# Performance work log

Measured on AMD Instinct MI355X. Metric: run time of the kernel, lower is better.

## Reference

```python
import jax, jax.numpy as jnp
import numpy as np

B, L, P, D = 2, 2048, 512, 4096
H, KH = 32, 8
HD = D // H  # 128
S = P + L


def setup_inputs() -> dict:
    key = jax.random.key(0)
    ks = jax.random.split(key, 8)
    x = jax.random.normal(ks[0], (B, L, D), dtype=jnp.float32)
    # causal mask accounting for past_len P: query i may attend keys j <= P + i
    qi = jnp.arange(L)[:, None]
    kj = jnp.arange(S)[None, :]
    mask = jnp.where(kj <= P + qi, 0.0, -1e9).astype(jnp.float32)[None, None]  # [1,1,L,S]
    past_k = jax.random.normal(ks[1], (B, KH, P, HD), dtype=jnp.float32)
    past_v = jax.random.normal(ks[2], (B, KH, P, HD), dtype=jnp.float32)
    scale = 0.02
    Wq = jax.random.normal(ks[3], (D, H * HD), dtype=jnp.float32) * scale
    Wk = jax.random.normal(ks[4], (D, KH * HD), dtype=jnp.float32) * scale
    Wv = jax.random.normal(ks[5], (D, KH * HD), dtype=jnp.float32) * scale
    Wo = jax.random.normal(ks[6], (D, D), dtype=jnp.float32) * scale
    return {"x": x, "mask": mask, "past_k": past_k, "past_v": past_v,
            "Wq": Wq, "Wk": Wk, "Wv": Wv, "Wo": Wo}


def reference(x, mask, past_k, past_v, Wq, Wk, Wv, Wo):
    b, l, d = x.shape
    # projections (nn.Linear with no bias: x @ W^T, here W stored already transposed)
    q = (x @ Wq).reshape(b, l, H, HD).transpose(0, 2, 1, 3)   # [B,H,L,hd]
    k = (x @ Wk).reshape(b, l, KH, HD).transpose(0, 2, 1, 3)  # [B,KH,L,hd]
    v = (x @ Wv).reshape(b, l, KH, HD).transpose(0, 2, 1, 3)
    # KV-cache concat along sequence dim
    k = jnp.concatenate([past_k, k], axis=2)  # [B,KH,S,hd]
    v = jnp.concatenate([past_v, v], axis=2)
    # GQA: repeat_interleave kv heads to match query heads
    g = H // KH
    k_rep = jnp.repeat(k, g, axis=1)  # [B,H,S,hd]
    v_rep = jnp.repeat(v, g, axis=1)
    scores = jnp.einsum('bhqd,bhkd->bhqk', q, k_rep) / (HD ** 0.5) + mask
    attn = jax.nn.softmax(scores, axis=-1)
    out = jnp.einsum('bhqk,bhkd->bhqd', attn, v_rep)
    out = out.transpose(0, 2, 1, 3).reshape(b, l, d) @ Wo
    return out
```

## Files before the change

### kernel.cpp

```cpp
#include <hip/hip_runtime.h>

using u16 = unsigned short;
using u32 = unsigned int;
using bf16x8 = __attribute__((ext_vector_type(8))) __bf16;
using f32x4  = __attribute__((ext_vector_type(4))) float;
using f32x16 = __attribute__((ext_vector_type(16))) float;
using u16x8  = __attribute__((ext_vector_type(8))) u16;
using u32x2  = __attribute__((ext_vector_type(2))) u32;

#define DEV static __device__ __forceinline__

DEV float bf2f(u16 u) { union { u32 i; float f; } c; c.i = ((u32)u) << 16; return c.f; }
DEV u16 f2bf(float f) {
  union { float f; u32 i; } c; c.f = f;
  u32 r = c.i + 0x7FFFu + ((c.i >> 16) & 1u);
  return (u16)(r >> 16);
}

DEV void gload_lds16(const void* g, void* l) {
  __builtin_amdgcn_global_load_lds(
      (const __attribute__((address_space(1))) u32*)g,
      (__attribute__((address_space(3))) u32*)l, 16, 0, 0);
}

DEV u32 cvtpk(float lo, float hi) {
  u32 r;
  asm("v_cvt_pk_bf16_f32 %0, %1, %2" : "=v"(r) : "v"(lo), "v"(hi));
  return r;
}
DEV void plswap(u32& a, u32& b) {
  auto r = __builtin_amdgcn_permlane32_swap((int)a, (int)b, false, false);
  a = (u32)r[0]; b = (u32)r[1];
}
DEV float crossmax(float x) {
  union { float f; u32 i; } c; c.f = x;
  u32 a = c.i, b = c.i;
  plswap(a, b);
  union { u32 i; float f; } A, B; A.i = a; B.i = b;
  return fmaxf(A.f, B.f);
}
DEV float crosssum(float x) {
  union { float f; u32 i; } c; c.f = x;
  u32 a = c.i, b = c.i;
  plswap(a, b);
  union { u32 i; float f; } A, B; A.i = a; B.i = b;
  return A.f + B.f;
}

DEV void fence_barrier() {
  asm volatile("" ::: "memory");
  __builtin_amdgcn_s_barrier();
  asm volatile("" ::: "memory");
}

__global__ __launch_bounds__(256) void cast_x_kernel(const float* __restrict__ x,
                                                     u16* __restrict__ xb) {
  size_t i = (size_t)blockIdx.x * 256 + threadIdx.x;
  const float4* s4 = (const float4*)(x + i * 8);
  float4 a = s4[0], c = s4[1];
  u16x8 o;
  o[0] = f2bf(a.x); o[1] = f2bf(a.y); o[2] = f2bf(a.z); o[3] = f2bf(a.w);
  o[4] = f2bf(c.x); o[5] = f2bf(c.y); o[6] = f2bf(c.z); o[7] = f2bf(c.w);
  *(u16x8*)(xb + i * 8) = o;
}

__global__ __launch_bounds__(256) void transpose_cast(const float* __restrict__ W,
                                                      u16* __restrict__ Wt, int K, int N) {
  __shared__ float t[32][33];
  int tx = threadIdx.x & 31, ty = threadIdx.x >> 5;
  int n0 = blockIdx.x * 32, k0 = blockIdx.y * 32;
#pragma unroll
  for (int i = 0; i < 4; ++i)
    t[ty + i * 8][tx] = W[(size_t)(k0 + ty + i * 8) * N + n0 + tx];
  __syncthreads();
#pragma unroll
  for (int i = 0; i < 4; ++i)
    Wt[(size_t)(n0 + ty + i * 8) * K + k0 + tx] = f2bf(t[tx][ty + i * 8]);
}


DEV int swap67(int p) { return (p & 63) | ((p & 64) << 1) | ((p & 128) >> 1); }
DEV int colmap(int p) { return (p & 31) | ((p & 96) << 1) | ((p >> 2) & 32); }

template <int PAR, int MH, int NH, bool VM, typename F>
DEV void gphase(const u16* lds, int wrp, int wcp, int c16, int g, int s7,
                f32x4 (&acc)[8][4], F&& stage) {
  bf16x8 af[4][2];
  bf16x8 bv[2][2];
#pragma unroll
  for (int fi = 0; fi < 4; ++fi) {
    const u16* rp = lds + PAR * 32768 + (MH * 128 + wrp + fi * 16 + c16) * 64;
    af[fi][0] = *(const bf16x8*)(rp + ((0 + g) ^ s7) * 8);
    af[fi][1] = *(const bf16x8*)(rp + ((4 + g) ^ s7) * 8);
  }
#pragma unroll
  for (int fj = 0; fj < 2; ++fj) {
    const u16* rp = lds + PAR * 32768 + 16384 + (NH * 128 + wcp + fj * 16 + c16) * 64;
    bv[fj][0] = *(const bf16x8*)(rp + ((0 + g) ^ s7) * 8);
    bv[fj][1] = *(const bf16x8*)(rp + ((4 + g) ^ s7) * 8);
  }
  stage();
  if (VM) asm volatile("s_waitcnt vmcnt(4)" ::: "memory");
  fence_barrier();
  __builtin_amdgcn_s_setprio(1);
#pragma unroll
  for (int fi = 0; fi < 4; ++fi)
#pragma unroll
    for (int fj = 0; fj < 2; ++fj) {
      acc[MH * 4 + fi][NH * 2 + fj] = __builtin_amdgcn_mfma_f32_16x16x32_bf16(
          af[fi][0], bv[fj][0], acc[MH * 4 + fi][NH * 2 + fj], 0, 0, 0);
      acc[MH * 4 + fi][NH * 2 + fj] = __builtin_amdgcn_mfma_f32_16x16x32_bf16(
          af[fi][1], bv[fj][1], acc[MH * 4 + fi][NH * 2 + fj], 0, 0, 0);
    }
  __builtin_amdgcn_s_setprio(0);
  fence_barrier();
}

template <typename CT>
__global__ __launch_bounds__(512, 2) void gemm8(const u16* __restrict__ A,
                                                const u16* __restrict__ Bt,
                                                CT* __restrict__ C, int M, int N, int K) {
  __shared__ u16 lds[65536];
  const int tid = threadIdx.x;
  const int w = tid >> 6, lane = tid & 63;
  const int g = lane >> 4, c16 = lane & 15, s7 = c16 & 7;
  const int nwg = gridDim.x * gridDim.y;
  const int bid0 = blockIdx.y * gridDim.x + blockIdx.x;
  const int sb = (bid0 & 7) * (nwg >> 3) + (bid0 >> 3);
  const int bn = (sb % gridDim.x) * 256;
  const int bm = (sb / gridDim.x) * 256;
  const int wr = (w >> 2) * 128, wc = (w & 3) * 64;
  const int wrp = (w >> 2) * 64, wcp = (w & 3) * 32;

  const int lr = lane >> 3;
  const int swz = ((lane & 7) ^ lr) * 8;
  u32 aOff[2][2], bOff[2][2];
#pragma unroll
  for (int h = 0; h < 2; ++h)
#pragma unroll
    for (int j = 0; j < 2; ++j) {
      int pb = h * 128 + (w * 2 + j) * 8;
      aOff[h][j] = (u32)(bm + swap67(pb) + lr) * (u32)K + swz;
      bOff[h][j] = (u32)(bn + colmap(pb) + lr) * (u32)K + swz;
    }
  auto stA = [&](int par, int h, int j, int ko) {
    gload_lds16(A + aOff[h][j] + ko, (u16*)lds + par * 32768 + h * 8192 + (w * 2 + j) * 512);
  };
  auto stB = [&](int par, int h, int j, int ko) {
    gload_lds16(Bt + bOff[h][j] + ko,
                (u16*)lds + par * 32768 + 16384 + h * 8192 + (w * 2 + j) * 512);
  };

  f32x4 acc[8][4] = {};

  stA(0, 0, 0, 0); stA(0, 0, 1, 0); stB(0, 0, 0, 0); stB(0, 0, 1, 0);
  stA(0, 1, 0, 0); stA(0, 1, 1, 0); stB(0, 1, 0, 0); stB(0, 1, 1, 0);
  stA(1, 0, 0, 64); stA(1, 0, 1, 64); stB(1, 0, 0, 64); stB(1, 0, 1, 64);
  asm volatile("s_waitcnt vmcnt(4)" ::: "memory");
  fence_barrier();

  for (int kb = 64; kb < K; kb += 128) {
    const int kc = kb + 64, kd = kb + 128;
    const bool hc = kc < K, hd = kd < K;
    gphase<0, 0, 0, false>(lds, wrp, wcp, c16, g, s7, acc, [&] {
      stA(1, 1, 0, kb); stA(1, 1, 1, kb); stB(1, 1, 0, kb); stB(1, 1, 1, kb);
    });
    gphase<0, 0, 1, false>(lds, wrp, wcp, c16, g, s7, acc, [&] {});
    gphase<0, 1, 0, false>(lds, wrp, wcp, c16, g, s7, acc, [&] {
      if (hc) { stA(0, 0, 0, kc); stA(0, 0, 1, kc); }
    });
    gphase<0, 1, 1, true>(lds, wrp, wcp, c16, g, s7, acc, [&] {
      if (hc) { stB(0, 0, 0, kc); stB(0, 0, 1, kc); }
    });
    gphase<1, 0, 0, false>(lds, wrp, wcp, c16, g, s7, acc, [&] {
      if (hc) { stA(0, 1, 0, kc); stA(0, 1, 1, kc); stB(0, 1, 0, kc); stB(0, 1, 1, kc); }
    });
    gphase<1, 0, 1, false>(lds, wrp, wcp, c16, g, s7, acc, [&] {});
    gphase<1, 1, 0, false>(lds, wrp, wcp, c16, g, s7, acc, [&] {
      if (hd) { stA(1, 0, 0, kd); stA(1, 0, 1, kd); }
    });
    gphase<1, 1, 1, true>(lds, wrp, wcp, c16, g, s7, acc, [&] {
      if (hd) { stB(1, 0, 0, kd); stB(1, 0, 1, kd); }
    });
  }

#pragma unroll
  for (int mf = 0; mf < 8; ++mf)
#pragma unroll
    for (int nf = 0; nf < 4; ++nf)
#pragma unroll
      for (int r = 0; r < 4; ++r) {
        int row = bm + wr + (mf >> 2) * 64 + (mf & 3) * 16 + g * 4 + r;
        int col = bn + wc + (nf >> 1) * 32 + (nf & 1) * 16 + c16;
        float v = acc[mf][nf][r];
        if constexpr (sizeof(CT) == 2) C[(size_t)row * N + col] = f2bf(v);
        else                           C[(size_t)row * N + col] = v;
      }
}

__global__ __launch_bounds__(256) void kcat(const float* __restrict__ past,
                                            const u16* __restrict__ kvb,
                                            u16* __restrict__ out) {
  int idx = blockIdx.x * 256 + threadIdx.x;
  int bkh = idx / 40960;
  int rem = idx - bkh * 40960;
  int s = rem >> 4;
  int d0 = (rem & 15) * 8;
  u16x8 o;
  if (s < 512) {
    const float4* s4 = (const float4*)(past + ((size_t)bkh * 512 + s) * 128 + d0);
    float4 a = s4[0], c = s4[1];
    o[0] = f2bf(a.x); o[1] = f2bf(a.y); o[2] = f2bf(a.z); o[3] = f2bf(a.w);
    o[4] = f2bf(c.x); o[5] = f2bf(c.y); o[6] = f2bf(c.z); o[7] = f2bf(c.w);
  } else {
    int b = bkh >> 3, khh = bkh & 7;
    o = *(const u16x8*)(kvb + (size_t)(b * 2048 + s - 512) * 2048 + khh * 128 + d0);
  }
  *(u16x8*)(out + (size_t)idx * 8) = o;
}

__global__ __launch_bounds__(256) void vt_build(const float* __restrict__ past,
                                                const u16* __restrict__ kvb,
                                                u16* __restrict__ vt) {
  __shared__ float t[32][33];
  int tx = threadIdx.x & 31, ty = threadIdx.x >> 5;
  int s0 = blockIdx.x * 32, d0 = blockIdx.y * 32, bkh = blockIdx.z;
  int b = bkh >> 3, khh = bkh & 7;
#pragma unroll
  for (int i = 0; i < 4; ++i) {
    int s = s0 + ty + i * 8;
    float v;
    if (s < 512) v = past[((size_t)bkh * 512 + s) * 128 + d0 + tx];
    else         v = bf2f(kvb[(size_t)(b * 2048 + s - 512) * 2048 + 1024 + khh * 128 + d0 + tx]);
    t[ty + i * 8][tx] = v;
  }
  __syncthreads();
#pragma unroll
  for (int i = 0; i < 4; ++i)
    vt[((size_t)bkh * 128 + d0 + ty + i * 8) * 2560 + s0 + tx] = f2bf(t[tx][ty + i * 8]);
}

__global__ __launch_bounds__(512, 2) void attn_fwd(const u16* __restrict__ Q,
                                                   const u16* __restrict__ Kc,
                                                   const u16* __restrict__ Vt,
                                                   u16* __restrict__ Oa) {
  __shared__ u16 lds[2][16384];
  const int tid = threadIdx.x;
  const int w = tid >> 6, lane = tid & 63;
  const int c32 = lane & 31, hi = lane >> 5;
  const int bid = blockIdx.x;
  const int b = bid >> 8;
  const int q8 = (bid >> 5) & 7;
  const int qt = b ? 7 - q8 : q8;
  const int h = bid & 31;
  const int kh = h >> 2;
  const int q0 = qt * 256;
  const int qw = q0 + w * 32;
  const int qg = qw + c32;
  const float SCALE = 0.08838834764831845f;

  bf16x8 qf[8];
  const u16* qbase = Q + (size_t)(b * 2048 + qg) * 4096 + h * 128 + hi * 8;
#pragma unroll
  for (int kc = 0; kc < 8; ++kc) qf[kc] = *(const bf16x8*)(qbase + kc * 16);

  const int krow = w * 4 + (lane >> 4);
  const int koff = krow * 128 + (((lane & 15) ^ (krow & 7)) * 8);
  const int vrow = w * 8 + (lane >> 3);
  const int voff = vrow * 2560 + (((lane & 7) ^ (vrow & 7)) * 8);
  const u16* kp = Kc + (size_t)(b * 8 + kh) * 2560 * 128;
  const u16* vp = Vt + (size_t)(b * 8 + kh) * 128 * 2560;
  u16* ksd0 = &lds[0][w * 512]; u16* ksd1 = &lds[1][w * 512];
  u16* vsd0 = &lds[0][8192 + w * 512]; u16* vsd1 = &lds[1][8192 + w * 512];

  const int ntiles = 4 * qt + 12;

  gload_lds16(kp + koff, ksd0);
  gload_lds16(kp + koff + 4096, ksd0 + 4096);
  gload_lds16(vp + voff, vsd0);
  gload_lds16(vp + voff + 163840, vsd0 + 4096);

  float m_run = -1e30f, l_run = 0.f;
  f32x16 oacc[4] = {};
  const int s7 = c32 & 7;

  for (int t = 0; t < ntiles; ++t) {
    const int pb = t & 1;
    if (t + 1 < ntiles) {
      u16* kd = pb ? ksd0 : ksd1;
      u16* vd = pb ? vsd0 : vsd1;
      gload_lds16(kp + 8192 + koff, kd);
      gload_lds16(kp + 8192 + koff + 4096, kd + 4096);
      gload_lds16(vp + 64 + voff, vd);
      gload_lds16(vp + 64 + voff + 163840, vd + 4096);
      asm volatile("s_waitcnt vmcnt(4)" ::: "memory");
    } else {
      asm volatile("s_waitcnt vmcnt(0)" ::: "memory");
    }
    __builtin_amdgcn_s_barrier();

    const int dd = 512 + qw - t * 64;
    if (dd >= -31) {
      const u16* Ks = &lds[pb][0];
      const u16* Vs = &lds[pb][8192];

      f32x16 sc[2] = {};
#pragma unroll
      for (int kc = 0; kc < 8; ++kc) {
#pragma unroll
        for (int sb = 0; sb < 2; ++sb) {
          const int sr = sb * 32 + c32;
          bf16x8 kf = *(const bf16x8*)(Ks + sr * 128 + (((kc * 2 + hi) ^ s7) * 8));
          sc[sb] = __builtin_amdgcn_mfma_f32_32x32x16_bf16(kf, qf[kc], sc[sb], 0, 0, 0);
        }
      }

      if (dd < 63) {
        const int base = 4 * hi - c32;
#pragma unroll
        for (int sb = 0; sb < 2; ++sb)
#pragma unroll
          for (int r = 0; r < 16; ++r) {
            const int srow = sb * 32 + (r & 3) + 8 * (r >> 2);
            if (srow + base > dd) sc[sb][r] = -1e30f;
          }
      }

      float pmax = -1e30f;
#pragma unroll
      for (int sb = 0; sb < 2; ++sb)
#pragma unroll
        for (int r = 0; r < 16; ++r) pmax = fmaxf(pmax, sc[sb][r]);
      pmax = crossmax(pmax);

      if (__any(pmax > m_run + 64.f)) {
        const float mn = fmaxf(m_run, pmax);
        const float corr = __expf((m_run - mn) * SCALE);
#pragma unroll
        for (int db = 0; db < 4; ++db)
#pragma unroll
          for (int r = 0; r < 16; ++r) oacc[db][r] *= corr;
        l_run *= corr;
        m_run = mn;
      }

      const float nms = -m_run * SCALE;
      float ls = 0.f;
#pragma unroll
      for (int sb = 0; sb < 2; ++sb)
#pragma unroll
        for (int r = 0; r < 16; ++r) {
          float p = __expf(fmaf(sc[sb][r], SCALE, nms));
          sc[sb][r] = p;
          ls += p;
        }
      l_run += crosssum(ls);

      bf16x8 pa[4];
#pragma unroll
      for (int c = 0; c < 4; ++c) {
        const int sb = c >> 1, bb = (c & 1) * 8;
        u32 a  = cvtpk(sc[sb][bb + 0], sc[sb][bb + 1]);
        u32 b2 = cvtpk(sc[sb][bb + 2], sc[sb][bb + 3]);
        u32 c2 = cvtpk(sc[sb][bb + 4], sc[sb][bb + 5]);
        u32 d2 = cvtpk(sc[sb][bb + 6], sc[sb][bb + 7]);
        plswap(a, c2);
        plswap(b2, d2);
        union { u32 u[4]; bf16x8 v; } cv;
        cv.u[0] = a; cv.u[1] = b2; cv.u[2] = c2; cv.u[3] = d2;
        pa[c] = cv.v;
      }

#pragma unroll
      for (int c = 0; c < 4; ++c) {
#pragma unroll
        for (int db = 0; db < 4; ++db) {
          const int d = db * 32 + c32;
          bf16x8 vf = *(const bf16x8*)(Vs + d * 64 + (((c * 2 + hi) ^ s7) * 8));
          oacc[db] = __builtin_amdgcn_mfma_f32_32x32x16_bf16(vf, pa[c], oacc[db], 0, 0, 0);
        }
      }
    }
    __builtin_amdgcn_s_barrier();
    kp += 8192; vp += 64;
  }

  const float linv = 1.f / l_run;
  u16* ob = Oa + (size_t)(b * 2048 + qg) * 4096 + h * 128 + 4 * hi;
#pragma unroll
  for (int db = 0; db < 4; ++db)
#pragma unroll
    for (int rg = 0; rg < 4; ++rg) {
      u32x2 st;
      st[0] = cvtpk(oacc[db][rg * 4 + 0] * linv, oacc[db][rg * 4 + 1] * linv);
      st[1] = cvtpk(oacc[db][rg * 4 + 2] * linv, oacc[db][rg * 4 + 3] * linv);
      *(u32x2*)(ob + db * 32 + rg * 8) = st;
    }
}

extern "C" void kernel_launch(void* const* d_in, const int* in_sizes, int n_in,
                              void* d_out, int out_size, void* d_ws, size_t ws_size,
                              hipStream_t stream) {
  (void)in_sizes; (void)n_in; (void)out_size; (void)ws_size;
  const float* x  = (const float*)d_in[0];
  const float* pk = (const float*)d_in[2];
  const float* pv = (const float*)d_in[3];
  const float* Wq = (const float*)d_in[4];
  const float* Wk = (const float*)d_in[5];
  const float* Wv = (const float*)d_in[6];
  const float* Wo = (const float*)d_in[7];
  float* out = (float*)d_out;

  char* w = (char*)d_ws;
  u16* xb  = (u16*)(w);
  u16* wt  = (u16*)(w + 33554432);
  u16* qb  = (u16*)(w + 67108864);
  u16* kvb = (u16*)(w + 100663296);
  u16* kc  = (u16*)(w + 117440512);
  u16* vt  = (u16*)(w + 127926272);
  u16* ao  = xb;

  cast_x_kernel<<<8192, 256, 0, stream>>>(x, xb);
  transpose_cast<<<dim3(128, 128), 256, 0, stream>>>(Wq, wt, 4096, 4096);
  gemm8<u16><<<dim3(16, 16), 512, 0, stream>>>(xb, wt, qb, 4096, 4096, 4096);
  transpose_cast<<<dim3(32, 128), 256, 0, stream>>>(Wk, wt, 4096, 1024);
  transpose_cast<<<dim3(32, 128), 256, 0, stream>>>(Wv, wt + (size_t)1024 * 4096, 4096, 1024);
  gemm8<u16><<<dim3(8, 16), 512, 0, stream>>>(xb, wt, kvb, 4096, 2048, 4096);
  kcat<<<2560, 256, 0, stream>>>(pk, kvb, kc);
  vt_build<<<dim3(80, 4, 16), 256, 0, stream>>>(pv, kvb, vt);
  transpose_cast<<<dim3(128, 128), 256, 0, stream>>>(Wo, wt, 4096, 4096);
  attn_fwd<<<512, 512, 0, stream>>>(qb, kc, vt, ao);
  gemm8<float><<<dim3(16, 16), 512, 0, stream>>>(ao, wt, out, 4096, 4096, 4096);
}
```

Before: 758.6 us.

## Split-K the KV projection GEMM and reuse LDS fragments across GEMM phases

After: 687.6 us. 9.4% less time.

```diff
diff --git a/kernel.cpp b/kernel.cpp
--- a/kernel.cpp
+++ b/kernel.cpp
@@ -82,22 +82,26 @@
 DEV int swap67(int p) { return (p & 63) | ((p & 64) << 1) | ((p & 128) >> 1); }
 DEV int colmap(int p) { return (p & 31) | ((p & 96) << 1) | ((p >> 2) & 32); }
 
-template <int PAR, int MH, int NH, bool VM, typename F>
+template <int PAR, int MH, int NH, bool LA, bool LB, bool VM, typename F>
 DEV void gphase(const u16* lds, int wrp, int wcp, int c16, int g, int s7,
-                f32x4 (&acc)[8][4], F&& stage) {
-  bf16x8 af[4][2];
-  bf16x8 bv[2][2];
-#pragma unroll
-  for (int fi = 0; fi < 4; ++fi) {
-    const u16* rp = lds + PAR * 32768 + (MH * 128 + wrp + fi * 16 + c16) * 64;
-    af[fi][0] = *(const bf16x8*)(rp + ((0 + g) ^ s7) * 8);
-    af[fi][1] = *(const bf16x8*)(rp + ((4 + g) ^ s7) * 8);
-  }
-#pragma unroll
-  for (int fj = 0; fj < 2; ++fj) {
-    const u16* rp = lds + PAR * 32768 + 16384 + (NH * 128 + wcp + fj * 16 + c16) * 64;
-    bv[fj][0] = *(const bf16x8*)(rp + ((0 + g) ^ s7) * 8);
-    bv[fj][1] = *(const bf16x8*)(rp + ((4 + g) ^ s7) * 8);
+                bf16x8 (&af)[4][2], bf16x8 (&bv)[2][2][2],
+                f32x4 (&acc)[8][4], bool pre_drain, F&& stage) {
+  if (pre_drain) asm volatile("s_waitcnt vmcnt(0)" ::: "memory");
+  if constexpr (LA) {
+#pragma unroll
+    for (int fi = 0; fi < 4; ++fi) {
+      const u16* rp = lds + PAR * 32768 + (MH * 128 + wrp + fi * 16 + c16) * 64;
+      af[fi][0] = *(const bf16x8*)(rp + ((0 + g) ^ s7) * 8);
+      af[fi][1] = *(const bf16x8*)(rp + ((4 + g) ^ s7) * 8);
+    }
+  }
+  if constexpr (LB) {
+#pragma unroll
+    for (int fj = 0; fj < 2; ++fj) {
+      const u16* rp = lds + PAR * 32768 + 16384 + (NH * 128 + wcp + fj * 16 + c16) * 64;
+      bv[NH][fj][0] = *(const bf16x8*)(rp + ((0 + g) ^ s7) * 8);
+      bv[NH][fj][1] = *(const bf16x8*)(rp + ((4 + g) ^ s7) * 8);
+    }
   }
   stage();
   if (VM) asm volatile("s_waitcnt vmcnt(4)" ::: "memory");
@@ -108,9 +112,9 @@
 #pragma unroll
     for (int fj = 0; fj < 2; ++fj) {
       acc[MH * 4 + fi][NH * 2 + fj] = __builtin_amdgcn_mfma_f32_16x16x32_bf16(
-          af[fi][0], bv[fj][0], acc[MH * 4 + fi][NH * 2 + fj], 0, 0, 0);
+          af[fi][0], bv[NH][fj][0], acc[MH * 4 + fi][NH * 2 + fj], 0, 0, 0);
       acc[MH * 4 + fi][NH * 2 + fj] = __builtin_amdgcn_mfma_f32_16x16x32_bf16(
-          af[fi][1], bv[fj][1], acc[MH * 4 + fi][NH * 2 + fj], 0, 0, 0);
+          af[fi][1], bv[NH][fj][1], acc[MH * 4 + fi][NH * 2 + fj], 0, 0, 0);
     }
   __builtin_amdgcn_s_setprio(0);
   fence_barrier();
@@ -119,11 +123,15 @@
 template <typename CT>
 __global__ __launch_bounds__(512, 2) void gemm8(const u16* __restrict__ A,
                                                 const u16* __restrict__ Bt,
-                                                CT* __restrict__ C, int M, int N, int K) {
+                                                CT* __restrict__ C, CT* __restrict__ C2,
+                                                int M, int N, int K, int lda) {
   __shared__ u16 lds[65536];
   const int tid = threadIdx.x;
   const int w = tid >> 6, lane = tid & 63;
   const int g = lane >> 4, c16 = lane & 15, s7 = c16 & 7;
+  A += (size_t)blockIdx.z * K;
+  Bt += (size_t)blockIdx.z * K;
+  CT* Cw = blockIdx.z ? C2 : C;
   const int nwg = gridDim.x * gridDim.y;
   const int bid0 = blockIdx.y * gridDim.x + blockIdx.x;
   const int sb = (bid0 & 7) * (nwg >> 3) + (bid0 >> 3);
@@ -140,8 +148,8 @@
 #pragma unroll
     for (int j = 0; j < 2; ++j) {
       int pb = h * 128 + (w * 2 + j) * 8;
-      aOff[h][j] = (u32)(bm + swap67(pb) + lr) * (u32)K + swz;
-      bOff[h][j] = (u32)(bn + colmap(pb) + lr) * (u32)K + swz;
+      aOff[h][j] = (u32)(bm + swap67(pb) + lr) * (u32)lda + swz;
+      bOff[h][j] = (u32)(bn + colmap(pb) + lr) * (u32)lda + swz;
     }
   auto stA = [&](int par, int h, int j, int ko) {
     gload_lds16(A + aOff[h][j] + ko, (u16*)lds + par * 32768 + h * 8192 + (w * 2 + j) * 512);
@@ -152,6 +160,8 @@
   };
 
   f32x4 acc[8][4] = {};
+  bf16x8 af[4][2];
+  bf16x8 bv[2][2][2];
 
   stA(0, 0, 0, 0); stA(0, 0, 1, 0); stB(0, 0, 0, 0); stB(0, 0, 1, 0);
   stA(0, 1, 0, 0); stA(0, 1, 1, 0); stB(0, 1, 0, 0); stB(0, 1, 1, 0);
@@ -162,24 +172,24 @@
   for (int kb = 64; kb < K; kb += 128) {
     const int kc = kb + 64, kd = kb + 128;
     const bool hc = kc < K, hd = kd < K;
-    gphase<0, 0, 0, false>(lds, wrp, wcp, c16, g, s7, acc, [&] {
+    gphase<0, 0, 0, true, true, false>(lds, wrp, wcp, c16, g, s7, af, bv, acc, false, [&] {
       stA(1, 1, 0, kb); stA(1, 1, 1, kb); stB(1, 1, 0, kb); stB(1, 1, 1, kb);
     });
-    gphase<0, 0, 1, false>(lds, wrp, wcp, c16, g, s7, acc, [&] {});
-    gphase<0, 1, 0, false>(lds, wrp, wcp, c16, g, s7, acc, [&] {
+    gphase<0, 0, 1, false, true, false>(lds, wrp, wcp, c16, g, s7, af, bv, acc, false, [&] {});
+    gphase<0, 1, 0, true, false, false>(lds, wrp, wcp, c16, g, s7, af, bv, acc, false, [&] {
       if (hc) { stA(0, 0, 0, kc); stA(0, 0, 1, kc); }
     });
-    gphase<0, 1, 1, true>(lds, wrp, wcp, c16, g, s7, acc, [&] {
+    gphase<0, 1, 1, false, false, true>(lds, wrp, wcp, c16, g, s7, af, bv, acc, false, [&] {
       if (hc) { stB(0, 0, 0, kc); stB(0, 0, 1, kc); }
     });
-    gphase<1, 0, 0, false>(lds, wrp, wcp, c16, g, s7, acc, [&] {
+    gphase<1, 0, 0, true, true, false>(lds, wrp, wcp, c16, g, s7, af, bv, acc, !hc, [&] {
       if (hc) { stA(0, 1, 0, kc); stA(0, 1, 1, kc); stB(0, 1, 0, kc); stB(0, 1, 1, kc); }
     });
-    gphase<1, 0, 1, false>(lds, wrp, wcp, c16, g, s7, acc, [&] {});
-    gphase<1, 1, 0, false>(lds, wrp, wcp, c16, g, s7, acc, [&] {
+    gphase<1, 0, 1, false, true, false>(lds, wrp, wcp, c16, g, s7, af, bv, acc, false, [&] {});
+    gphase<1, 1, 0, true, false, false>(lds, wrp, wcp, c16, g, s7, af, bv, acc, false, [&] {
       if (hd) { stA(1, 0, 0, kd); stA(1, 0, 1, kd); }
     });
-    gphase<1, 1, 1, true>(lds, wrp, wcp, c16, g, s7, acc, [&] {
+    gphase<1, 1, 1, false, false, true>(lds, wrp, wcp, c16, g, s7, af, bv, acc, false, [&] {
       if (hd) { stB(1, 0, 0, kd); stB(1, 0, 1, kd); }
     });
   }
@@ -193,13 +203,14 @@
         int row = bm + wr + (mf >> 2) * 64 + (mf & 3) * 16 + g * 4 + r;
         int col = bn + wc + (nf >> 1) * 32 + (nf & 1) * 16 + c16;
         float v = acc[mf][nf][r];
-        if constexpr (sizeof(CT) == 2) C[(size_t)row * N + col] = f2bf(v);
-        else                           C[(size_t)row * N + col] = v;
+        if constexpr (sizeof(CT) == 2) Cw[(size_t)row * N + col] = f2bf(v);
+        else                           Cw[(size_t)row * N + col] = v;
       }
 }
 
 __global__ __launch_bounds__(256) void kcat(const float* __restrict__ past,
                                             const u16* __restrict__ kvb,
+                                            const u16* __restrict__ kvb2,
                                             u16* __restrict__ out) {
   int idx = blockIdx.x * 256 + threadIdx.x;
   int bkh = idx / 40960;
@@ -214,13 +225,18 @@
     o[4] = f2bf(c.x); o[5] = f2bf(c.y); o[6] = f2bf(c.z); o[7] = f2bf(c.w);
   } else {
     int b = bkh >> 3, khh = bkh & 7;
-    o = *(const u16x8*)(kvb + (size_t)(b * 2048 + s - 512) * 2048 + khh * 128 + d0);
+    size_t off = (size_t)(b * 2048 + s - 512) * 2048 + khh * 128 + d0;
+    u16x8 k1 = *(const u16x8*)(kvb + off);
+    u16x8 k2 = *(const u16x8*)(kvb2 + off);
+#pragma unroll
+    for (int j = 0; j < 8; ++j) o[j] = f2bf(bf2f(k1[j]) + bf2f(k2[j]));
   }
   *(u16x8*)(out + (size_t)idx * 8) = o;
 }
 
 __global__ __launch_bounds__(256) void vt_build(const float* __restrict__ past,
                                                 const u16* __restrict__ kvb,
+                                                const u16* __restrict__ kvb2,
                                                 u16* __restrict__ vt) {
   __shared__ float t[32][33];
   int tx = threadIdx.x & 31, ty = threadIdx.x >> 5;
@@ -230,8 +246,12 @@
   for (int i = 0; i < 4; ++i) {
     int s = s0 + ty + i * 8;
     float v;
-    if (s < 512) v = past[((size_t)bkh * 512 + s) * 128 + d0 + tx];
-    else         v = bf2f(kvb[(size_t)(b * 2048 + s - 512) * 2048 + 1024 + khh * 128 + d0 + tx]);
+    if (s < 512) {
+      v = past[((size_t)bkh * 512 + s) * 128 + d0 + tx];
+    } else {
+      size_t off = (size_t)(b * 2048 + s - 512) * 2048 + 1024 + khh * 128 + d0 + tx;
+      v = bf2f(kvb[off]) + bf2f(kvb2[off]);
+    }
     t[ty + i * 8][tx] = v;
   }
   __syncthreads();
@@ -412,23 +432,24 @@
   float* out = (float*)d_out;
 
   char* w = (char*)d_ws;
-  u16* xb  = (u16*)(w);
-  u16* wt  = (u16*)(w + 33554432);
-  u16* qb  = (u16*)(w + 67108864);
-  u16* kvb = (u16*)(w + 100663296);
-  u16* kc  = (u16*)(w + 117440512);
-  u16* vt  = (u16*)(w + 127926272);
-  u16* ao  = xb;
+  u16* xb   = (u16*)(w);
+  u16* wt   = (u16*)(w + 33554432);
+  u16* kvb2 = (u16*)(w + 50331648);
+  u16* qb   = (u16*)(w + 67108864);
+  u16* kvb  = (u16*)(w + 100663296);
+  u16* kc   = (u16*)(w + 117440512);
+  u16* vt   = (u16*)(w + 127926272);
+  u16* ao   = xb;
 
   cast_x_kernel<<<8192, 256, 0, stream>>>(x, xb);
   transpose_cast<<<dim3(128, 128), 256, 0, stream>>>(Wq, wt, 4096, 4096);
-  gemm8<u16><<<dim3(16, 16), 512, 0, stream>>>(xb, wt, qb, 4096, 4096, 4096);
+  gemm8<u16><<<dim3(16, 16), 512, 0, stream>>>(xb, wt, qb, qb, 4096, 4096, 4096, 4096);
   transpose_cast<<<dim3(32, 128), 256, 0, stream>>>(Wk, wt, 4096, 1024);
   transpose_cast<<<dim3(32, 128), 256, 0, stream>>>(Wv, wt + (size_t)1024 * 4096, 4096, 1024);
-  gemm8<u16><<<dim3(8, 16), 512, 0, stream>>>(xb, wt, kvb, 4096, 2048, 4096);
-  kcat<<<2560, 256, 0, stream>>>(pk, kvb, kc);
-  vt_build<<<dim3(80, 4, 16), 256, 0, stream>>>(pv, kvb, vt);
+  gemm8<u16><<<dim3(8, 16, 2), 512, 0, stream>>>(xb, wt, kvb, kvb2, 4096, 2048, 2048, 4096);
+  kcat<<<2560, 256, 0, stream>>>(pk, kvb, kvb2, kc);
+  vt_build<<<dim3(80, 4, 16), 256, 0, stream>>>(pv, kvb, kvb2, vt);
   transpose_cast<<<dim3(128, 128), 256, 0, stream>>>(Wo, wt, 4096, 4096);
   attn_fwd<<<512, 512, 0, stream>>>(qb, kc, vt, ao);
-  gemm8<float><<<dim3(16, 16), 512, 0, stream>>>(ao, wt, out, 4096, 4096, 4096);
-}
+  gemm8<float><<<dim3(16, 16), 512, 0, stream>>>(ao, wt, out, out, 4096, 4096, 4096, 4096);
+}
```
